# Optimization experiments

Measured on AMD Instinct MI355X. Metric: run time of the kernel, lower is better.

The kernel has to match this reference:

```python
import jax, jax.numpy as jnp
import numpy as np
from jax import lax

V, H, L, F = 50304, 512, 6, 2048
SKIP_INTERVAL = 1
B, S = 4, 1024


def layer_norm(x, w, b, eps=1e-5):
    mu = jnp.mean(x, axis=-1, keepdims=True)
    var = jnp.mean(jnp.square(x - mu), axis=-1, keepdims=True)
    return (x - mu) * lax.rsqrt(var + eps) * w + b


def setup_inputs() -> dict:
    key = jax.random.key(0)
    ks = jax.random.split(key, 8)
    s = 0.02
    return {
        "input_ids": jax.random.randint(ks[0], (B, S), 0, V, dtype=jnp.int64),
        "embed_in": jax.random.normal(ks[1], (V, H), jnp.float32) * s,
        "hp_w": jax.random.normal(ks[2], (H, H), jnp.float32) * s,
        "hp_b": jnp.zeros((H,), jnp.float32),
        "ln_w": jnp.ones((L, H), jnp.float32),
        "ln_b": jnp.zeros((L, H), jnp.float32),
        "W1": jax.random.normal(ks[3], (L, H, F), jnp.float32) * s,
        "b1": jnp.zeros((L, F), jnp.float32),
        "W2": jax.random.normal(ks[4], (L, F, H), jnp.float32) * s,
        "b2": jnp.zeros((L, H), jnp.float32),
        "ln_f_w": jnp.ones((H,), jnp.float32),
        "ln_f_b": jnp.zeros((H,), jnp.float32),
        "embed_out_w": jax.random.normal(ks[5], (V, H), jnp.float32) * s,
    }


def _stack(h, ln_w, ln_b, W1, b1, W2, b2):
    # scan over L layers; each is pre-LN residual MLP: h + gelu(LN(h) @ W1 + b1) @ W2 + b2
    def step(h, p):
        lw, lb, w1, bb1, w2, bb2 = p
        y = layer_norm(h, lw, lb)
        h = h + jnp.dot(jax.nn.gelu(jnp.dot(y, w1) + bb1), w2) + bb2
        return h, None
    h, _ = lax.scan(step, h, (ln_w, ln_b, W1, b1, W2, b2))
    return h


def reference(input_ids, embed_in, hp_w, hp_b, ln_w, ln_b, W1, b1, W2, b2, ln_f_w, ln_f_b, embed_out_w):
    # forward_selective with attention_mask=None and stateless layers is
    # position-independent, so the token loop vectorizes exactly to [B,S,H].
    h = embed_in[input_ids]  # [B,S,H] gather
    h = _stack(h, ln_w, ln_b, W1, b1, W2, b2)
    for _ in range(SKIP_INTERVAL):
        h = jnp.dot(h, hp_w.T) + hp_b  # hidden_proj
        h = _stack(h, ln_w, ln_b, W1, b1, W2, b2)
    normed = layer_norm(h, ln_f_w, ln_f_b)
    logits = jnp.dot(normed, embed_out_w.T)  # [B,S,V]
    final_hidden = h[:, -1, :]  # [B,H]
    return logits, final_hidden
```

## Files before the change

kernel.cpp:

```cpp
#include <hip/hip_runtime.h>
#include <hip/hip_bf16.h>
#include <cstdint>

using bf16 = __hip_bfloat16;
typedef __bf16 bf16x8 __attribute__((ext_vector_type(8)));
typedef float f32x4 __attribute__((ext_vector_type(4)));

constexpr int Hd = 512;
constexpr int Ld = 6;
constexpr int Fd = 2048;
constexpr int Vd = 50304;
constexpr int Md = 4096;

__device__ __forceinline__ unsigned short f2b(float x) {
  return __builtin_bit_cast(unsigned short, __float2bfloat16(x));
}

__device__ __forceinline__ float gelu_tanh(float x) {
  const float c = 0.7978845608028654f;
  float x3 = x * x * x;
  return 0.5f * x * (1.0f + tanhf(c * (x + 0.044715f * x3)));
}

__device__ __forceinline__ void load16_lds(const bf16* g, bf16* l) {
  __builtin_amdgcn_global_load_lds(
      (const __attribute__((address_space(1))) void*)g,
      (__attribute__((address_space(3))) void*)l, 16, 0, 0);
}

__global__ __launch_bounds__(256) void cast8(const float* __restrict__ in,
                                             bf16* __restrict__ out, int n8) {
  int i = blockIdx.x * 256 + threadIdx.x;
  if (i >= n8) return;
  const float4* p = (const float4*)in;
  float4 a = p[2 * i], b = p[2 * i + 1];
  uint4 o = {(unsigned)f2b(a.x) | ((unsigned)f2b(a.y) << 16),
             (unsigned)f2b(a.z) | ((unsigned)f2b(a.w) << 16),
             (unsigned)f2b(b.x) | ((unsigned)f2b(b.y) << 16),
             (unsigned)f2b(b.z) | ((unsigned)f2b(b.w) << 16)};
  ((uint4*)out)[i] = o;
}

__global__ void transpose_cast(const float* __restrict__ in, bf16* __restrict__ out,
                               int R, int C) {
  __shared__ float tile[32][33];
  int l = blockIdx.z;
  in += (size_t)l * R * C;
  out += (size_t)l * R * C;
  int c0 = blockIdx.x * 32, r0 = blockIdx.y * 32;
#pragma unroll
  for (int i = 0; i < 4; i++) {
    int r = r0 + threadIdx.y + i * 8;
    tile[threadIdx.y + i * 8][threadIdx.x] = in[(size_t)r * C + c0 + threadIdx.x];
  }
  __syncthreads();
#pragma unroll
  for (int i = 0; i < 4; i++) {
    int c = c0 + threadIdx.y + i * 8;
    out[(size_t)c * R + r0 + threadIdx.x] = (bf16)tile[threadIdx.x][threadIdx.y + i * 8];
  }
}

__global__ void gather_embed(const int* __restrict__ ids, const float* __restrict__ emb,
                             float* __restrict__ h) {
  int row = blockIdx.x;
  int id = ids[row];
  const float4* src = (const float4*)(emb + (size_t)id * Hd);
  float4* dst = (float4*)(h + (size_t)row * Hd);
  dst[threadIdx.x] = src[threadIdx.x];
}

template <int MODE>
__global__ __launch_bounds__(256) void ln_rows(
    const float* __restrict__ h, const float* __restrict__ p0,
    const float* __restrict__ p1, const float* __restrict__ fb,
    const float* __restrict__ w, const float* __restrict__ b,
    float* __restrict__ hout, bf16* __restrict__ y) {
  int row = blockIdx.x * 4 + (threadIdx.x >> 6);
  int lane = threadIdx.x & 63;
  size_t base = (size_t)row * Hd + lane * 8;
  float xv[8];
  if constexpr (MODE == 0) {
    *(float4*)&xv[0] = *(const float4*)(h + base);
    *(float4*)&xv[4] = *(const float4*)(h + base + 4);
  } else {
    float4 q0 = *(const float4*)(p0 + base), q1 = *(const float4*)(p0 + base + 4);
    float4 r0 = *(const float4*)(p1 + base), r1 = *(const float4*)(p1 + base + 4);
    float4 f0 = *(const float4*)(fb + lane * 8), f1 = *(const float4*)(fb + lane * 8 + 4);
    xv[0] = q0.x + r0.x + f0.x; xv[1] = q0.y + r0.y + f0.y;
    xv[2] = q0.z + r0.z + f0.z; xv[3] = q0.w + r0.w + f0.w;
    xv[4] = q1.x + r1.x + f1.x; xv[5] = q1.y + r1.y + f1.y;
    xv[6] = q1.z + r1.z + f1.z; xv[7] = q1.w + r1.w + f1.w;
    if constexpr (MODE == 1) {
      float4 a0 = *(const float4*)(h + base), a1 = *(const float4*)(h + base + 4);
      xv[0] += a0.x; xv[1] += a0.y; xv[2] += a0.z; xv[3] += a0.w;
      xv[4] += a1.x; xv[5] += a1.y; xv[6] += a1.z; xv[7] += a1.w;
    }
    *(float4*)(hout + base) = make_float4(xv[0], xv[1], xv[2], xv[3]);
    *(float4*)(hout + base + 4) = make_float4(xv[4], xv[5], xv[6], xv[7]);
  }
  float s = 0.f;
#pragma unroll
  for (int j = 0; j < 8; j++) s += xv[j];
#pragma unroll
  for (int off = 1; off < 64; off <<= 1) s += __shfl_xor(s, off);
  float mu = s * (1.0f / 512.0f);
  float s2 = 0.f;
#pragma unroll
  for (int j = 0; j < 8; j++) {
    xv[j] -= mu;
    s2 += xv[j] * xv[j];
  }
#pragma unroll
  for (int off = 1; off < 64; off <<= 1) s2 += __shfl_xor(s2, off);
  float scale = rsqrtf(s2 * (1.0f / 512.0f) + 1e-5f);
  float o[8];
#pragma unroll
  for (int j = 0; j < 8; j++) {
    float wj = w[lane * 8 + j], bj = b[lane * 8 + j];
    o[j] = xv[j] * scale * wj + bj;
  }
  uint4 pk = {(unsigned)f2b(o[0]) | ((unsigned)f2b(o[1]) << 16),
              (unsigned)f2b(o[2]) | ((unsigned)f2b(o[3]) << 16),
              (unsigned)f2b(o[4]) | ((unsigned)f2b(o[5]) << 16),
              (unsigned)f2b(o[6]) | ((unsigned)f2b(o[7]) << 16)};
  *(uint4*)(y + base) = pk;
}

__global__ __launch_bounds__(256) void finish2(
    const float* __restrict__ p0, const float* __restrict__ p1,
    const float* __restrict__ fb, float* __restrict__ h, bf16* __restrict__ hbf) {
  int i = blockIdx.x * 256 + threadIdx.x;
  size_t base = (size_t)i * 8;
  int col = (int)(base & 511);
  float x[8];
#pragma unroll
  for (int j = 0; j < 8; j += 4) {
    float4 a = *(const float4*)(h + base + j);
    float4 q = *(const float4*)(p0 + base + j);
    float4 r = *(const float4*)(p1 + base + j);
    float4 f = *(const float4*)(fb + col + j);
    x[j] = a.x + q.x + r.x + f.x; x[j + 1] = a.y + q.y + r.y + f.y;
    x[j + 2] = a.z + q.z + r.z + f.z; x[j + 3] = a.w + q.w + r.w + f.w;
    *(float4*)(h + base + j) = make_float4(x[j], x[j + 1], x[j + 2], x[j + 3]);
  }
  uint4 pk = {(unsigned)f2b(x[0]) | ((unsigned)f2b(x[1]) << 16),
              (unsigned)f2b(x[2]) | ((unsigned)f2b(x[3]) << 16),
              (unsigned)f2b(x[4]) | ((unsigned)f2b(x[5]) << 16),
              (unsigned)f2b(x[6]) | ((unsigned)f2b(x[7]) << 16)};
  *(uint4*)(hbf + base) = pk;
}

template <int EPI, int BN, bool MSWZ>
__global__ __launch_bounds__(256) void gemm_bt(
    const bf16* __restrict__ A, const bf16* __restrict__ Bt,
    const float* __restrict__ bias, float* __restrict__ outF,
    bf16* __restrict__ outB, int M, int N, int Klen, int lda, int ldb) {
  constexpr int ASZ = 128 * 32;
  constexpr int BSZ = BN * 32;
  constexpr int TILE = ASZ + BSZ;
  __shared__ bf16 lds[2 * TILE];
  const int tid = threadIdx.x;
  const int wave = tid >> 6;
  const int lane = tid & 63;
  constexpr int NF = BN / 32;
  const int wm = (wave >> 1) * 64;
  const int wn = (wave & 1) * (BN / 2);

  int bm, bn;
  if constexpr (MSWZ) {
    const int per = gridDim.x >> 3;
    const int wg = (blockIdx.x & 7) * per + (blockIdx.x >> 3);
    const int nM = M >> 7;
    bm = wg & (nM - 1);
    bn = wg / nM;
  } else {
    bn = blockIdx.x;
    bm = blockIdx.y;
  }
  const int rowA0 = bm * 128;
  const int rowB0 = bn * BN;
  const int k0 = blockIdx.z * Klen;

  const bf16* srcA[2];
#pragma unroll
  for (int r = 0; r < 2; r++) {
    int c = (r * 4 + wave) * 64 + lane;
    srcA[r] = A + (size_t)(rowA0 + (c >> 2)) * lda + k0 + (c & 3) * 8;
  }
  const bf16* srcB[BN / 64];
#pragma unroll
  for (int r = 0; r < BN / 64; r++) {
    int c = (r * 4 + wave) * 64 + lane;
    srcB[r] = Bt + (size_t)(rowB0 + (c >> 2)) * ldb + k0 + (c & 3) * 8;
  }

  f32x4 acc[4][NF];
#pragma unroll
  for (int i = 0; i < 4; i++)
#pragma unroll
    for (int j = 0; j < NF; j++) acc[i][j] = (f32x4){0.f, 0.f, 0.f, 0.f};

  const int fr = lane & 15;
  const int ko = (lane >> 4) * 8;

  auto STAGE = [&](int buf) {
    bf16* dst = lds + buf * TILE;
#pragma unroll
    for (int r = 0; r < 2; r++) {
      load16_lds(srcA[r], dst + (r * 4 + wave) * 512);
      srcA[r] += 32;
    }
#pragma unroll
    for (int r = 0; r < BN / 64; r++) {
      load16_lds(srcB[r], dst + ASZ + (r * 4 + wave) * 512);
      srcB[r] += 32;
    }
  };

  STAGE(0);
  __syncthreads();
  const int nIter = Klen >> 5;
  for (int it = 0; it < nIter; ++it) {
    const int cur = it & 1;
    if (it + 1 < nIter) STAGE(cur ^ 1);
    const bf16* lA = lds + cur * TILE;
    const bf16* lB = lA + ASZ;
    bf16x8 af[4], bfr[NF];
#pragma unroll
    for (int f = 0; f < 4; f++)
      af[f] = *(const bf16x8*)(lA + (wm + f * 16 + fr) * 32 + ko);
#pragma unroll
    for (int f = 0; f < NF; f++)
      bfr[f] = *(const bf16x8*)(lB + (wn + f * 16 + fr) * 32 + ko);
#pragma unroll
    for (int i = 0; i < 4; i++)
#pragma unroll
      for (int j = 0; j < NF; j++)
        acc[i][j] = __builtin_amdgcn_mfma_f32_16x16x32_bf16(af[i], bfr[j], acc[i][j], 0, 0, 0);
    __syncthreads();
  }

  if constexpr (EPI == 4) outF += (size_t)blockIdx.z * M * N;
  const int orow = (lane >> 4) * 4;
  const int ocol = lane & 15;
#pragma unroll
  for (int i = 0; i < 4; i++) {
#pragma unroll
    for (int j = 0; j < NF; j++) {
      int row0 = rowA0 + wm + i * 16 + orow;
      int col = rowB0 + wn + j * 16 + ocol;
#pragma unroll
      for (int q = 0; q < 4; q++) {
        float v = acc[i][j][q];
        size_t idx = (size_t)(row0 + q) * N + col;
        if constexpr (EPI == 0) {
          outB[idx] = (bf16)gelu_tanh(v + bias[col]);
        } else {
          outF[idx] = v;
        }
      }
    }
  }
}

template <int EPI, bool MSWZ>
__global__ __launch_bounds__(512) void gemm_bt256(
    const bf16* __restrict__ A, const bf16* __restrict__ Bt,
    const float* __restrict__ bias, float* __restrict__ outF,
    bf16* __restrict__ outB, int M, int N, int lda, int ldb) {
  constexpr int ASZ = 256 * 32;
  constexpr int BSZ = 128 * 32;
  constexpr int TILE = ASZ + BSZ;
  __shared__ bf16 lds[2 * TILE];
  const int tid = threadIdx.x;
  const int wave = tid >> 6;
  const int lane = tid & 63;
  const int wm = (wave >> 1) * 64;
  const int wn = (wave & 1) * 64;

  int bm, bn;
  if constexpr (MSWZ) {
    const int per = gridDim.x >> 3;
    const int wg = (blockIdx.x & 7) * per + (blockIdx.x >> 3);
    const int nM = M >> 8;
    bm = wg & (nM - 1);
    bn = wg / nM;
  } else {
    bn = blockIdx.x;
    bm = blockIdx.y;
  }
  const int rowA0 = bm * 256;
  const int rowB0 = bn * 128;

  const bf16* srcA[2];
#pragma unroll
  for (int r = 0; r < 2; r++) {
    int c = r * 512 + tid;
    srcA[r] = A + (size_t)(rowA0 + (c >> 2)) * lda + (c & 3) * 8;
  }
  int cB = tid;
  const bf16* srcB = Bt + (size_t)(rowB0 + (cB >> 2)) * ldb + (cB & 3) * 8;

  f32x4 acc[4][4];
#pragma unroll
  for (int i = 0; i < 4; i++)
#pragma unroll
    for (int j = 0; j < 4; j++) acc[i][j] = (f32x4){0.f, 0.f, 0.f, 0.f};

  const int fr = lane & 15;
  const int ko = (lane >> 4) * 8;

  auto STAGE = [&](int buf) {
    bf16* dst = lds + buf * TILE;
#pragma unroll
    for (int r = 0; r < 2; r++) {
      load16_lds(srcA[r], dst + (r * 512 + tid) * 8);
      srcA[r] += 32;
    }
    load16_lds(srcB, dst + ASZ + tid * 8);
    srcB += 32;
  };

  STAGE(0);
  __syncthreads();
  const int nIter = 512 >> 5;
  for (int it = 0; it < nIter; ++it) {
    const int cur = it & 1;
    if (it + 1 < nIter) STAGE(cur ^ 1);
    const bf16* lA = lds + cur * TILE;
    const bf16* lB = lA + ASZ;
    bf16x8 af[4], bfr[4];
#pragma unroll
    for (int f = 0; f < 4; f++)
      af[f] = *(const bf16x8*)(lA + (wm + f * 16 + fr) * 32 + ko);
#pragma unroll
    for (int f = 0; f < 4; f++)
      bfr[f] = *(const bf16x8*)(lB + (wn + f * 16 + fr) * 32 + ko);
#pragma unroll
    for (int i = 0; i < 4; i++)
#pragma unroll
      for (int j = 0; j < 4; j++)
        acc[i][j] = __builtin_amdgcn_mfma_f32_16x16x32_bf16(af[i], bfr[j], acc[i][j], 0, 0, 0);
    __syncthreads();
  }

  const int orow = (lane >> 4) * 4;
  const int ocol = lane & 15;
#pragma unroll
  for (int i = 0; i < 4; i++) {
#pragma unroll
    for (int j = 0; j < 4; j++) {
      int row0 = rowA0 + wm + i * 16 + orow;
      int col = rowB0 + wn + j * 16 + ocol;
#pragma unroll
      for (int q = 0; q < 4; q++) {
        float v = acc[i][j][q];
        size_t idx = (size_t)(row0 + q) * N + col;
        if constexpr (EPI == 0) {
          outB[idx] = (bf16)gelu_tanh(v + bias[col]);
        } else {
          outF[idx] = v;
        }
      }
    }
  }
}

__global__ void tail_copy(const float* __restrict__ h, float* __restrict__ out) {
  int t = blockIdx.x * 256 + threadIdx.x;
  int b = t >> 9, k = t & 511;
  out[t] = h[((size_t)(b * 1024 + 1023)) * Hd + k];
}

extern "C" void kernel_launch(void* const* d_in, const int* in_sizes, int n_in,
                              void* d_out, int out_size, void* d_ws, size_t ws_size,
                              hipStream_t stream) {
  const int* ids = (const int*)d_in[0];
  const float* emb = (const float*)d_in[1];
  const float* hp_w = (const float*)d_in[2];
  const float* hp_b = (const float*)d_in[3];
  const float* ln_w = (const float*)d_in[4];
  const float* ln_b = (const float*)d_in[5];
  const float* W1 = (const float*)d_in[6];
  const float* b1 = (const float*)d_in[7];
  const float* W2 = (const float*)d_in[8];
  const float* b2 = (const float*)d_in[9];
  const float* lnf_w = (const float*)d_in[10];
  const float* lnf_b = (const float*)d_in[11];
  const float* eow = (const float*)d_in[12];
  float* out = (float*)d_out;

  char* ws = (char*)d_ws;
  float* h = (float*)(ws);
  bf16* ybf = (bf16*)(ws + (8u << 20));
  bf16* abf = (bf16*)(ws + (12u << 20));
  bf16* W1t = (bf16*)(ws + (28u << 20));
  bf16* W2t = (bf16*)(ws + (40u << 20));
  bf16* hpwB = (bf16*)(ws + (52u << 20));
  bf16* eowB = (bf16*)(ws + (53u << 20));

  float* p0 = out;
  float* p1 = out + (size_t)Md * Hd;

  cast8<<<dim3(Vd * Hd / 8 / 256), dim3(256), 0, stream>>>(eow, eowB, Vd * Hd / 8);
  cast8<<<dim3(Hd * Hd / 8 / 256), dim3(256), 0, stream>>>(hp_w, hpwB, Hd * Hd / 8);
  transpose_cast<<<dim3(Fd / 32, Hd / 32, Ld), dim3(32, 8), 0, stream>>>(W1, W1t, Hd, Fd);
  transpose_cast<<<dim3(Hd / 32, Fd / 32, Ld), dim3(32, 8), 0, stream>>>(W2, W2t, Fd, Hd);

  gather_embed<<<dim3(Md), dim3(128), 0, stream>>>(ids, emb, h);

  auto layer = [&](int l, int mode, const float* fb, const float* lw, const float* lb) {
    if (mode == 0)
      ln_rows<0><<<dim3(Md / 4), dim3(256), 0, stream>>>(h, p0, p1, fb, lw, lb, h, ybf);
    else if (mode == 1)
      ln_rows<1><<<dim3(Md / 4), dim3(256), 0, stream>>>(h, p0, p1, fb, lw, lb, h, ybf);
    else
      ln_rows<2><<<dim3(Md / 4), dim3(256), 0, stream>>>(h, p0, p1, fb, lw, lb, h, ybf);
    gemm_bt256<0, false><<<dim3(Fd / 128, Md / 256), dim3(512), 0, stream>>>(
        ybf, W1t + (size_t)l * Fd * Hd, b1 + (size_t)l * Fd, (float*)nullptr, abf,
        Md, Fd, Hd, Hd);
    gemm_bt<4, 64, false><<<dim3(Hd / 64, Md / 128, 2), dim3(256), 0, stream>>>(
        abf, W2t + (size_t)l * Hd * Fd, (const float*)nullptr, p0, (bf16*)nullptr,
        Md, Hd, Fd / 2, Fd, Fd);
  };

  layer(0, 0, nullptr, ln_w, ln_b);
  for (int l = 1; l < Ld; l++)
    layer(l, 1, b2 + (size_t)(l - 1) * Hd, ln_w + (size_t)l * Hd, ln_b + (size_t)l * Hd);
  finish2<<<dim3(Md * Hd / 8 / 256), dim3(256), 0, stream>>>(
      p0, p1, b2 + (size_t)(Ld - 1) * Hd, h, ybf);

  gemm_bt<4, 64, false><<<dim3(Hd / 64, Md / 128, 2), dim3(256), 0, stream>>>(
      ybf, hpwB, (const float*)nullptr, p0, (bf16*)nullptr, Md, Hd, Hd / 2, Hd, Hd);

  layer(0, 2, hp_b, ln_w, ln_b);
  for (int l = 1; l < Ld; l++)
    layer(l, 1, b2 + (size_t)(l - 1) * Hd, ln_w + (size_t)l * Hd, ln_b + (size_t)l * Hd);

  ln_rows<1><<<dim3(Md / 4), dim3(256), 0, stream>>>(
      h, p0, p1, b2 + (size_t)(Ld - 1) * Hd, lnf_w, lnf_b, h, ybf);
  gemm_bt256<3, true><<<dim3((Vd / 128) * (Md / 256)), dim3(512), 0, stream>>>(
      ybf, eowB, (const float*)nullptr, out, (bf16*)nullptr, Md, Vd, Hd, Hd);

  tail_copy<<<dim3(8), dim3(256), 0, stream>>>(h, out + (size_t)Md * Vd);
}
```

Measured before the change: 1.092 ms.

## Triple-buffer GEMM LDS staging with explicit vmcnt waits and single barrier

Both bf16 GEMM kernels move from double-buffered to triple-buffered LDS staging. Loads run two K-steps ahead. Each iteration now uses one barrier, preceded by a partial s_waitcnt vmcnt, instead of two __syncthreads. This should hide more global-to-LDS latency and cut barrier stalls. In exchange it uses more LDS per block, which may lower occupancy, and correctness depends on the hand-counted vmcnt values matching the number of outstanding loads per stage.

```diff
diff --git a/kernel.cpp b/kernel.cpp
--- a/kernel.cpp
+++ b/kernel.cpp
@@ -159,7 +159,7 @@
   constexpr int ASZ = 128 * 32;
   constexpr int BSZ = BN * 32;
   constexpr int TILE = ASZ + BSZ;
-  __shared__ bf16 lds[2 * TILE];
+  __shared__ bf16 lds[3 * TILE];
   const int tid = threadIdx.x;
   const int wave = tid >> 6;
   const int lane = tid & 63;
@@ -204,8 +204,8 @@
   const int fr = lane & 15;
   const int ko = (lane >> 4) * 8;
 
-  auto STAGE = [&](int buf) {
-    bf16* dst = lds + buf * TILE;
+  auto STAGE = [&](int slot) {
+    bf16* dst = lds + slot * TILE;
 #pragma unroll
     for (int r = 0; r < 2; r++) {
       load16_lds(srcA[r], dst + (r * 4 + wave) * 512);
@@ -219,11 +219,21 @@
   };
 
   STAGE(0);
-  __syncthreads();
+  STAGE(1);
   const int nIter = Klen >> 5;
+  int cur = 0, stg = 2;
   for (int it = 0; it < nIter; ++it) {
-    const int cur = it & 1;
-    if (it + 1 < nIter) STAGE(cur ^ 1);
+    if (it < nIter - 1) {
+      if constexpr (BN == 64)
+        asm volatile("s_waitcnt vmcnt(3)" ::: "memory");
+      else
+        asm volatile("s_waitcnt vmcnt(4)" ::: "memory");
+    } else {
+      asm volatile("s_waitcnt vmcnt(0)" ::: "memory");
+    }
+    __builtin_amdgcn_s_barrier();
+    __builtin_amdgcn_sched_barrier(0);
+    if (it + 2 < nIter) STAGE(stg);
     const bf16* lA = lds + cur * TILE;
     const bf16* lB = lA + ASZ;
     bf16x8 af[4], bfr[NF];
@@ -238,7 +248,8 @@
 #pragma unroll
       for (int j = 0; j < NF; j++)
         acc[i][j] = __builtin_amdgcn_mfma_f32_16x16x32_bf16(af[i], bfr[j], acc[i][j], 0, 0, 0);
-    __syncthreads();
+    cur = (cur == 2) ? 0 : cur + 1;
+    stg = (stg == 2) ? 0 : stg + 1;
   }
 
   if constexpr (EPI == 4) outF += (size_t)blockIdx.z * M * N;
@@ -272,7 +283,7 @@
   constexpr int ASZ = 256 * 32;
   constexpr int BSZ = 128 * 32;
   constexpr int TILE = ASZ + BSZ;
-  __shared__ bf16 lds[2 * TILE];
+  __shared__ bf16 lds[3 * TILE];
   const int tid = threadIdx.x;
   const int wave = tid >> 6;
   const int lane = tid & 63;
@@ -311,8 +322,8 @@
   const int fr = lane & 15;
   const int ko = (lane >> 4) * 8;
 
-  auto STAGE = [&](int buf) {
-    bf16* dst = lds + buf * TILE;
+  auto STAGE = [&](int slot) {
+    bf16* dst = lds + slot * TILE;
 #pragma unroll
     for (int r = 0; r < 2; r++) {
       load16_lds(srcA[r], dst + (r * 512 + tid) * 8);
@@ -323,11 +334,17 @@
   };
 
   STAGE(0);
-  __syncthreads();
+  STAGE(1);
   const int nIter = 512 >> 5;
+  int cur = 0, stg = 2;
   for (int it = 0; it < nIter; ++it) {
-    const int cur = it & 1;
-    if (it + 1 < nIter) STAGE(cur ^ 1);
+    if (it < nIter - 1)
+      asm volatile("s_waitcnt vmcnt(3)" ::: "memory");
+    else
+      asm volatile("s_waitcnt vmcnt(0)" ::: "memory");
+    __builtin_amdgcn_s_barrier();
+    __builtin_amdgcn_sched_barrier(0);
+    if (it + 2 < nIter) STAGE(stg);
     const bf16* lA = lds + cur * TILE;
     const bf16* lB = lA + ASZ;
     bf16x8 af[4], bfr[4];
@@ -342,7 +359,8 @@
 #pragma unroll
       for (int j = 0; j < 4; j++)
         acc[i][j] = __builtin_amdgcn_mfma_f32_16x16x32_bf16(af[i], bfr[j], acc[i][j], 0, 0, 0);
-    __syncthreads();
+    cur = (cur == 2) ? 0 : cur + 1;
+    stg = (stg == 2) ? 0 : stg + 1;
   }
 
   const int orow = (lane >> 4) * 4;
```

After: 1.078 ms. About the same (-1.3%).
